# Kernel tuning notes

Hardware: AMD Instinct MI355X
Metric: run time of the kernel (lower is better)

The kernel has to match this reference:

```python
import jax, jax.numpy as jnp
import numpy as np

TEMPERATURE = 0.5


def setup_inputs() -> dict:
    key = jax.random.key(0)
    k1, k2 = jax.random.split(key)
    z_i = jax.random.normal(k1, (4096, 256), dtype=jnp.float32)
    z_j = jax.random.normal(k2, (4096, 256), dtype=jnp.float32)
    return {"z_i": z_i, "z_j": z_j}


def _l2norm(x, eps=1e-12):
    n = jnp.sqrt(jnp.sum(x * x, axis=1, keepdims=True))
    return x / jnp.maximum(n, eps)


def reference(z_i, z_j):
    n = z_i.shape[0]
    zi = _l2norm(z_i)
    zj = _l2norm(z_j)
    reps = jnp.concatenate([zi, zj], axis=0)            # [2N, D], rows unit-norm
    # cosine similarity of unit vectors == dot product -> normalized GEMM
    sim = jnp.matmul(reps, reps.T)                      # [2N, 2N]
    sim_ij = jnp.diagonal(sim, offset=n)                # [N]
    sim_ji = jnp.diagonal(sim, offset=-n)               # [N]
    positives = jnp.concatenate([sim_ij, sim_ji], axis=0)  # [2N]
    mask = 1.0 - jnp.eye(2 * n, dtype=sim.dtype)
    numerator = jnp.exp(positives / TEMPERATURE)
    denominator = jnp.sum(mask * jnp.exp(sim / TEMPERATURE), axis=1)
    loss = -jnp.log(numerator / denominator)
    return jnp.mean(loss)
```

## Files before the change

kernel.cpp:

```cpp
#include <hip/hip_runtime.h>
#include <hip/hip_bf16.h>


#define D      256
#define KC     8
#define RT     4
#define BM     256
#define BN     64
#define NSPLIT 16
#define CEXP   2.885390081777926f
#define E2     7.38905609893065f
#define FBLK   32

typedef __bf16 bf16x8 __attribute__((ext_vector_type(8)));
typedef float  f32x4  __attribute__((ext_vector_type(4)));
typedef __attribute__((address_space(1))) const unsigned int* gas_t;
typedef __attribute__((address_space(3))) unsigned int*       las_t;

static __device__ __forceinline__ void gload_lds16(const void* g, void* l) {
    __builtin_amdgcn_global_load_lds((gas_t)(uintptr_t)g, (las_t)(uintptr_t)l, 16, 0, 0);
}

static __device__ __forceinline__ unsigned short f2bf(float x) {
    union { float f; unsigned u; } v; v.f = x;
    unsigned r = v.u + 0x7fffu + ((v.u >> 16) & 1u);
    return (unsigned short)(r >> 16);
}

__global__ __launch_bounds__(64) void knorm(const float* __restrict__ zi,
                                            const float* __restrict__ zj,
                                            unsigned short* __restrict__ reps,
                                            float* __restrict__ pos, int n) {
    const int i = blockIdx.x;
    const int lane = threadIdx.x;
    const float4 a = ((const float4*)(zi + (size_t)i * D))[lane];
    const float4 b = ((const float4*)(zj + (size_t)i * D))[lane];
    float si = a.x*a.x + a.y*a.y + a.z*a.z + a.w*a.w;
    float sj = b.x*b.x + b.y*b.y + b.z*b.z + b.w*b.w;
    float sd = a.x*b.x + a.y*b.y + a.z*b.z + a.w*b.w;
    #pragma unroll
    for (int off = 32; off; off >>= 1) {
        si += __shfl_xor(si, off);
        sj += __shfl_xor(sj, off);
        sd += __shfl_xor(sd, off);
    }
    const float inv_i = 1.0f / fmaxf(sqrtf(si), 1e-12f);
    const float inv_j = 1.0f / fmaxf(sqrtf(sj), 1e-12f);
    if (lane == 0) pos[i] = sd * inv_i * inv_j;
    ushort4 pa, pb;
    pa.x = f2bf(a.x * inv_i); pa.y = f2bf(a.y * inv_i);
    pa.z = f2bf(a.z * inv_i); pa.w = f2bf(a.w * inv_i);
    pb.x = f2bf(b.x * inv_j); pb.y = f2bf(b.y * inv_j);
    pb.z = f2bf(b.z * inv_j); pb.w = f2bf(b.w * inv_j);
    ((ushort4*)(reps + (size_t)i * D))[lane]       = pa;
    ((ushort4*)(reps + (size_t)(i + n) * D))[lane] = pb;
}

__global__ __launch_bounds__(256, 2) void krowsum(const unsigned short* __restrict__ reps,
                                                  float* __restrict__ partial, int twoN) {
    __shared__ unsigned short buf[2][BN * D];
    const int lane  = threadIdx.x & 63;
    const int rbase = blockIdx.x * BM + (threadIdx.x >> 6) * (RT * 16);
    const int seg   = twoN / NSPLIT;
    const int cb0   = blockIdx.y * seg;
    const int lrow  = lane & 15;
    const int lkb   = (lane >> 4) * 16;
    const int swz   = (lrow & 7) << 4;
    const int NCH   = seg / BN;

    bf16x8 afrag[RT][KC];
    #pragma unroll
    for (int rt = 0; rt < RT; ++rt) {
        const char* ar = (const char*)(reps + (size_t)(rbase + rt * 16 + lrow) * D) + lkb;
        #pragma unroll
        for (int kc = 0; kc < KC; ++kc)
            afrag[rt][kc] = *(const bf16x8*)(ar + kc * 64);
    }

    float rs[RT][4];
    #pragma unroll
    for (int rt = 0; rt < RT; ++rt)
        #pragma unroll
        for (int e = 0; e < 4; ++e) rs[rt][e] = 0.f;

    #define STAGE(b, c)                                                           \
        do {                                                                      \
            const char* src_ = (const char*)(reps + (size_t)(cb0 + (c) * BN) * D);\
            _Pragma("unroll")                                                     \
            for (int i_ = 0; i_ < 8; ++i_) {                                      \
                int o_   = i_ * 4096 + threadIdx.x * 16;                          \
                int row_ = o_ >> 9;                                               \
                int cb_  = o_ & 511;                                              \
                gload_lds16(src_ + row_ * 512 + (cb_ ^ ((row_ & 7) << 4)),        \
                            (char*)(&buf[(b)][0]) + o_);                          \
            }                                                                     \
        } while (0)

    STAGE(0, 0);
    __syncthreads();
    int cur = 0;
    for (int c = 0; c < NCH; ++c) {
        if (c + 1 < NCH) STAGE(cur ^ 1, c + 1);
        const char* bb = (const char*)(&buf[cur][0]);
        #pragma unroll
        for (int tp = 0; tp < 2; ++tp) {
            f32x4 acc[RT][2];
            #pragma unroll
            for (int rt = 0; rt < RT; ++rt) {
                acc[rt][0] = (f32x4){0.f, 0.f, 0.f, 0.f};
                acc[rt][1] = (f32x4){0.f, 0.f, 0.f, 0.f};
            }
            #pragma unroll
            for (int kc = 0; kc < KC; ++kc) {
                const int kb = (kc * 64 + lkb) ^ swz;
                bf16x8 bf0 = *(const bf16x8*)(bb + ((tp * 2 + 0) * 16 + lrow) * 512 + kb);
                bf16x8 bf1 = *(const bf16x8*)(bb + ((tp * 2 + 1) * 16 + lrow) * 512 + kb);
                #pragma unroll
                for (int rt = 0; rt < RT; ++rt) {
                    acc[rt][0] = __builtin_amdgcn_mfma_f32_16x16x32_bf16(
                        afrag[rt][kc], bf0, acc[rt][0], 0, 0, 0);
                    acc[rt][1] = __builtin_amdgcn_mfma_f32_16x16x32_bf16(
                        afrag[rt][kc], bf1, acc[rt][1], 0, 0, 0);
                }
            }
            #pragma unroll
            for (int rt = 0; rt < RT; ++rt)
                #pragma unroll
                for (int e = 0; e < 4; ++e)
                    rs[rt][e] += __builtin_amdgcn_exp2f(acc[rt][0][e] * CEXP)
                               + __builtin_amdgcn_exp2f(acc[rt][1][e] * CEXP);
        }
        __syncthreads();
        cur ^= 1;
    }

    #pragma unroll
    for (int rt = 0; rt < RT; ++rt)
        #pragma unroll
        for (int e = 0; e < 4; ++e)
            #pragma unroll
            for (int off = 1; off < 16; off <<= 1)
                rs[rt][e] += __shfl_xor(rs[rt][e], off);
    if ((lane & 15) == 0) {
        #pragma unroll
        for (int rt = 0; rt < RT; ++rt) {
            const int rg = rbase + rt * 16 + (lane >> 4) * 4;
            #pragma unroll
            for (int e = 0; e < 4; ++e)
                partial[(size_t)(rg + e) * NSPLIT + blockIdx.y] = rs[rt][e];
        }
    }
}

__global__ __launch_bounds__(256) void kfinal1(const float* __restrict__ partial,
                                               const float* __restrict__ pos,
                                               float* __restrict__ bsum,
                                               int twoN, int n) {
    __shared__ float red[256];
    const int r = blockIdx.x * 256 + threadIdx.x;
    float s = 0.f;
    if (r < twoN) {
        const f32x4* pr = (const f32x4*)(partial + (size_t)r * NSPLIT);
        f32x4 v = pr[0];
        #pragma unroll
        for (int q = 1; q < NSPLIT / 4; ++q) {
            f32x4 u = pr[q];
            v[0] += u[0]; v[1] += u[1]; v[2] += u[2]; v[3] += u[3];
        }
        float dsum = (v[0] + v[1]) + (v[2] + v[3]) - E2;
        const float p = pos[r < n ? r : r - n];
        s = logf(dsum) - 2.0f * p;
    }
    red[threadIdx.x] = s;
    __syncthreads();
    #pragma unroll
    for (int off = 128; off; off >>= 1) {
        if (threadIdx.x < off) red[threadIdx.x] += red[threadIdx.x + off];
        __syncthreads();
    }
    if (threadIdx.x == 0) bsum[blockIdx.x] = red[0];
}

__global__ __launch_bounds__(64) void kfinal2(const float* __restrict__ bsum,
                                              float* __restrict__ out, int twoN) {
    float s = threadIdx.x < FBLK ? bsum[threadIdx.x] : 0.f;
    #pragma unroll
    for (int off = 32; off; off >>= 1) s += __shfl_xor(s, off);
    if (threadIdx.x == 0) out[0] = s / (float)twoN;
}

extern "C" void kernel_launch(void* const* d_in, const int* in_sizes, int n_in,
                              void* d_out, int out_size, void* d_ws, size_t ws_size,
                              hipStream_t stream) {
    const float* zi = (const float*)d_in[0];
    const float* zj = (const float*)d_in[1];
    const int n    = in_sizes[0] / D;
    const int twoN = 2 * n;

    unsigned short* reps = (unsigned short*)d_ws;
    float* pos     = (float*)((char*)d_ws + (size_t)twoN * D * 2);
    float* partial = pos + n;
    float* bsum    = partial + (size_t)twoN * NSPLIT;
    float* out     = (float*)d_out;

    knorm<<<n, 64, 0, stream>>>(zi, zj, reps, pos, n);
    dim3 gridB(twoN / BM, NSPLIT);
    krowsum<<<gridB, 256, 0, stream>>>(reps, partial, twoN);
    kfinal1<<<FBLK, 256, 0, stream>>>(partial, pos, bsum, twoN, n);
    kfinal2<<<1, 64, 0, stream>>>(bsum, out, twoN);
}
```

Measured before the change: 49.70 us.

## Exploit symmetry of similarity matrix by computing only upper-triangular tile pairs

The similarity matrix is symmetric, so the row-sum kernel now computes only upper-triangular 256x256 panel pairs, 528 blocks instead of 512 blocks of the full grid. Each off-diagonal block also accumulates column sums of the exp values through LDS and writes them as the partial for the mirrored rows. This roughly halves the MFMA and exp work. In exchange it adds column-sum shuffles and LDS traffic, loads the A fragments by staging through LDS, and widens the partial array to 32 slots, which makes the final reduction read more.

New measurement: 89.11 us. 1.79x slower.

```diff
diff --git a/kernel.cpp b/kernel.cpp
--- a/kernel.cpp
+++ b/kernel.cpp
@@ -5,9 +5,10 @@
 #define D      256
 #define KC     8
 #define RT     4
-#define BM     256
+#define PAN    32
+#define NBLK   (PAN * (PAN + 1) / 2)
 #define BN     64
-#define NSPLIT 16
+#define SLOTS  32
 #define CEXP   2.885390081777926f
 #define E2     7.38905609893065f
 #define FBLK   32
@@ -26,6 +27,31 @@
     unsigned r = v.u + 0x7fffu + ((v.u >> 16) & 1u);
     return (unsigned short)(r >> 16);
 }
+
+#define STAGE(bufp, srcp)                                                 \
+    do {                                                                  \
+        const char* s_ = (const char*)(srcp);                             \
+        char* d_ = (char*)(bufp);                                         \
+        _Pragma("unroll")                                                 \
+        for (int i_ = 0; i_ < 8; ++i_) {                                  \
+            int o_   = i_ * 4096 + threadIdx.x * 16;                      \
+            int row_ = o_ >> 9;                                           \
+            int cb_  = o_ & 511;                                          \
+            gload_lds16(s_ + row_ * 512 + (cb_ ^ ((row_ & 7) << 4)),      \
+                        d_ + o_);                                         \
+        }                                                                 \
+    } while (0)
+
+#define LOAD_AFRAG(srcbase)                                               \
+    do {                                                                  \
+        const char* ab_ = (const char*)(srcbase);                         \
+        _Pragma("unroll")                                                 \
+        for (int rt_ = 0; rt_ < RT; ++rt_)                                \
+            _Pragma("unroll")                                             \
+            for (int kc_ = 0; kc_ < KC; ++kc_)                            \
+                afrag[rt_][kc_] = *(const bf16x8*)(ab_ +                  \
+                    (rt_ * 16 + lrow) * 512 + ((kc_ * 64 + lkb) ^ swz));  \
+    } while (0)
 
 __global__ __launch_bounds__(64) void knorm(const float* __restrict__ zi,
                                             const float* __restrict__ zj,
@@ -57,25 +83,32 @@
 }
 
 __global__ __launch_bounds__(256, 2) void krowsum(const unsigned short* __restrict__ reps,
-                                                  float* __restrict__ partial, int twoN) {
+                                                  float* __restrict__ partial) {
     __shared__ unsigned short buf[2][BN * D];
-    const int lane  = threadIdx.x & 63;
-    const int rbase = blockIdx.x * BM + (threadIdx.x >> 6) * (RT * 16);
-    const int seg   = twoN / NSPLIT;
-    const int cb0   = blockIdx.y * seg;
-    const int lrow  = lane & 15;
-    const int lkb   = (lane >> 4) * 16;
-    const int swz   = (lrow & 7) << 4;
-    const int NCH   = seg / BN;
+    __shared__ float cs_lds[4][16][16];
+    const int lane = threadIdx.x & 63;
+    const int w    = threadIdx.x >> 6;
+    const int lrow = lane & 15;
+    const int lkb  = (lane >> 4) * 16;
+    const int swz  = (lrow & 7) << 4;
+
+    int bid = blockIdx.x, rpan = 0, rem = PAN;
+    while (bid >= rem) { bid -= rem; ++rpan; --rem; }
+    const int cpan = rpan + bid;
+    const bool diag = (rpan == cpan);
 
     bf16x8 afrag[RT][KC];
-    #pragma unroll
-    for (int rt = 0; rt < RT; ++rt) {
-        const char* ar = (const char*)(reps + (size_t)(rbase + rt * 16 + lrow) * D) + lkb;
-        #pragma unroll
-        for (int kc = 0; kc < KC; ++kc)
-            afrag[rt][kc] = *(const bf16x8*)(ar + kc * 64);
-    }
+    const char* Ab = (const char*)reps + (size_t)rpan * 256 * 512;
+    STAGE(&buf[0][0], Ab);
+    STAGE(&buf[1][0], Ab + 32768);
+    __syncthreads();
+    if (w < 2) LOAD_AFRAG(&buf[w][0]);
+    __syncthreads();
+    STAGE(&buf[0][0], Ab + 2 * 32768);
+    STAGE(&buf[1][0], Ab + 3 * 32768);
+    __syncthreads();
+    if (w >= 2) LOAD_AFRAG(&buf[w - 2][0]);
+    __syncthreads();
 
     float rs[RT][4];
     #pragma unroll
@@ -83,25 +116,14 @@
         #pragma unroll
         for (int e = 0; e < 4; ++e) rs[rt][e] = 0.f;
 
-    #define STAGE(b, c)                                                           \
-        do {                                                                      \
-            const char* src_ = (const char*)(reps + (size_t)(cb0 + (c) * BN) * D);\
-            _Pragma("unroll")                                                     \
-            for (int i_ = 0; i_ < 8; ++i_) {                                      \
-                int o_   = i_ * 4096 + threadIdx.x * 16;                          \
-                int row_ = o_ >> 9;                                               \
-                int cb_  = o_ & 511;                                              \
-                gload_lds16(src_ + row_ * 512 + (cb_ ^ ((row_ & 7) << 4)),        \
-                            (char*)(&buf[(b)][0]) + o_);                          \
-            }                                                                     \
-        } while (0)
-
-    STAGE(0, 0);
+    const char* Bb = (const char*)reps + (size_t)cpan * 256 * 512;
+    STAGE(&buf[0][0], Bb);
     __syncthreads();
     int cur = 0;
-    for (int c = 0; c < NCH; ++c) {
-        if (c + 1 < NCH) STAGE(cur ^ 1, c + 1);
-        const char* bb = (const char*)(&buf[cur][0]);
+    for (int c = 0; c < 4; ++c) {
+        if (c < 3) STAGE(&buf[cur ^ 1][0], Bb + (size_t)(c + 1) * 32768);
+        const char* bb = (const char*)&buf[cur][0];
+        float cs0 = 0.f, cs1 = 0.f, cs2 = 0.f, cs3 = 0.f;
         #pragma unroll
         for (int tp = 0; tp < 2; ++tp) {
             f32x4 acc[RT][2];
@@ -126,9 +148,25 @@
             #pragma unroll
             for (int rt = 0; rt < RT; ++rt)
                 #pragma unroll
-                for (int e = 0; e < 4; ++e)
-                    rs[rt][e] += __builtin_amdgcn_exp2f(acc[rt][0][e] * CEXP)
-                               + __builtin_amdgcn_exp2f(acc[rt][1][e] * CEXP);
+                for (int e = 0; e < 4; ++e) {
+                    float e0 = __builtin_amdgcn_exp2f(acc[rt][0][e] * CEXP);
+                    float e1 = __builtin_amdgcn_exp2f(acc[rt][1][e] * CEXP);
+                    rs[rt][e] += e0 + e1;
+                    if (tp == 0) { cs0 += e0; cs1 += e1; }
+                    else         { cs2 += e0; cs3 += e1; }
+                }
+        }
+        if (!diag) {
+            cs0 += __shfl_xor(cs0, 16); cs0 += __shfl_xor(cs0, 32);
+            cs1 += __shfl_xor(cs1, 16); cs1 += __shfl_xor(cs1, 32);
+            cs2 += __shfl_xor(cs2, 16); cs2 += __shfl_xor(cs2, 32);
+            cs3 += __shfl_xor(cs3, 16); cs3 += __shfl_xor(cs3, 32);
+            if (lane < 16) {
+                cs_lds[w][c * 4 + 0][lane] = cs0;
+                cs_lds[w][c * 4 + 1][lane] = cs1;
+                cs_lds[w][c * 4 + 2][lane] = cs2;
+                cs_lds[w][c * 4 + 3][lane] = cs3;
+            }
         }
         __syncthreads();
         cur ^= 1;
@@ -141,14 +179,24 @@
             #pragma unroll
             for (int off = 1; off < 16; off <<= 1)
                 rs[rt][e] += __shfl_xor(rs[rt][e], off);
+    const int rbase = rpan * 256 + w * 64;
     if ((lane & 15) == 0) {
         #pragma unroll
         for (int rt = 0; rt < RT; ++rt) {
             const int rg = rbase + rt * 16 + (lane >> 4) * 4;
             #pragma unroll
             for (int e = 0; e < 4; ++e)
-                partial[(size_t)(rg + e) * NSPLIT + blockIdx.y] = rs[rt][e];
-        }
+                partial[(size_t)(rg + e) * SLOTS + cpan] = rs[rt][e];
+        }
+    }
+
+    if (!diag) {
+        const int ct  = threadIdx.x >> 4;
+        const int col = threadIdx.x & 15;
+        const float v = cs_lds[0][ct][col] + cs_lds[1][ct][col]
+                      + cs_lds[2][ct][col] + cs_lds[3][ct][col];
+        const int gcol = cpan * 256 + (ct >> 2) * 64 + (ct & 3) * 16 + col;
+        partial[(size_t)gcol * SLOTS + rpan] = v;
     }
 }
 
@@ -160,10 +208,10 @@
     const int r = blockIdx.x * 256 + threadIdx.x;
     float s = 0.f;
     if (r < twoN) {
-        const f32x4* pr = (const f32x4*)(partial + (size_t)r * NSPLIT);
+        const f32x4* pr = (const f32x4*)(partial + (size_t)r * SLOTS);
         f32x4 v = pr[0];
         #pragma unroll
-        for (int q = 1; q < NSPLIT / 4; ++q) {
+        for (int q = 1; q < SLOTS / 4; ++q) {
             f32x4 u = pr[q];
             v[0] += u[0]; v[1] += u[1]; v[2] += u[2]; v[3] += u[3];
         }
@@ -200,12 +248,11 @@
     unsigned short* reps = (unsigned short*)d_ws;
     float* pos     = (float*)((char*)d_ws + (size_t)twoN * D * 2);
     float* partial = pos + n;
-    float* bsum    = partial + (size_t)twoN * NSPLIT;
+    float* bsum    = partial + (size_t)twoN * SLOTS;
     float* out     = (float*)d_out;
 
     knorm<<<n, 64, 0, stream>>>(zi, zj, reps, pos, n);
-    dim3 gridB(twoN / BM, NSPLIT);
-    krowsum<<<gridB, 256, 0, stream>>>(reps, partial, twoN);
+    krowsum<<<NBLK, 256, 0, stream>>>(reps, partial);
     kfinal1<<<FBLK, 256, 0, stream>>>(partial, pos, bsum, twoN, n);
     kfinal2<<<1, 64, 0, stream>>>(bsum, out, twoN);
 }
```
